# Optimization experiments

Measured on AMD Instinct MI355X. Metric: run time of the kernel, lower is better.

## Reference

```python
import jax, jax.numpy as jnp
import numpy as np

WH, WW = 7, 7
N = WH * WW
NH = 6
HEAD_DIM = 192 // NH
W_RES = 56
R_MAX = 4 * 56  # patch_size[0] * H
PI = 3.141592653589793


def _rel_coords():
    ch, cw = np.arange(WH), np.arange(WW)
    coords = np.stack(np.meshgrid(ch, cw, indexing='ij'))  # (2, WH, WW)
    flat = coords.reshape(2, -1)
    rel = flat[:, :, None] - flat[:, None, :]  # (2, N, N)
    radius = rel[0]   # in [-(WH-1), WH-1]
    azimuth = rel[1]  # in [-(WW-1), WW-1]
    return radius, azimuth


def setup_inputs() -> dict:
    key = jax.random.key(0)
    ks = jax.random.split(key, 10)
    B_ = 2048
    dim = 192
    return {
        'x': jax.random.normal(ks[0], (B_, N, dim), jnp.float32),
        'D': jax.random.uniform(ks[1], (B_, 1), jnp.float32),
        'qkv_w': jax.random.normal(ks[2], (3 * dim, dim), jnp.float32) * 0.02,
        'qkv_b': jax.random.normal(ks[3], (3 * dim,), jnp.float32) * 0.02,
        'proj_w': jax.random.normal(ks[4], (dim, dim), jnp.float32) * 0.02,
        'proj_b': jax.random.normal(ks[5], (dim,), jnp.float32) * 0.02,
        'a_p': jax.random.normal(ks[6], (2 * WW - 1, NH), jnp.float32) * 0.02,
        'b_p': jax.random.normal(ks[7], (2 * WW - 1, NH), jnp.float32) * 0.02,
        'a_r': jax.random.normal(ks[8], (2 * WH - 1, NH), jnp.float32) * 0.02,
        'b_r': jax.random.normal(ks[9], (2 * WH - 1, NH), jnp.float32) * 0.02,
    }


def reference(x, D, qkv_w, qkv_b, proj_w, proj_b, a_p, b_p, a_r, b_r):
    B_, n, C = x.shape
    radius_np, azimuth_np = _rel_coords()
    # torch a_r[radius] with negative ints wraps like python indexing; emulate via modulo
    rad_idx = jnp.asarray(radius_np % (2 * WH - 1))
    az_idx = jnp.asarray(azimuth_np % (2 * WW - 1))
    radius = jnp.asarray(radius_np, jnp.float32)   # (N, N)
    azimuth = jnp.asarray(azimuth_np, jnp.float32)  # (N, N)

    scale = HEAD_DIM ** -0.5
    qkv = (x @ qkv_w.T + qkv_b).reshape(B_, n, 3, NH, HEAD_DIM)
    qkv = jnp.transpose(qkv, (2, 0, 3, 1, 4))  # (3, B_, NH, N, hd)
    q, k, v = qkv[0] * scale, qkv[1], qkv[2]

    attn = jnp.einsum('bhnd,bhmd->bhnm', q, k)  # (B_, NH, N, N)

    # azimuthal bias: (N, N, NH) -> (NH, N, N)
    az = azimuth * (2.0 * PI / W_RES)
    A_phi = a_p[az_idx] * jnp.cos(az)[..., None] + b_p[az_idx] * jnp.sin(az)[..., None]
    A_phi = jnp.transpose(A_phi, (2, 0, 1))  # (NH, N, N)

    # radial bias: D (B_,1) scales radius -> (B_, N, N); combine -> (B_, NH, N, N)
    rad = D[:, 0][:, None, None] * radius[None]  # (B_, N, N)
    ang = rad * (2.0 * PI / R_MAX)
    A_r = (a_r[rad_idx][None] * jnp.cos(ang)[..., None]
           + b_r[rad_idx][None] * jnp.sin(ang)[..., None])  # (B_, N, N, NH)
    A_r = jnp.transpose(A_r, (0, 3, 1, 2))  # (B_, NH, N, N)

    attn = jax.nn.softmax(attn + A_phi[None] + A_r, axis=-1)
    out = jnp.einsum('bhnm,bhmd->bhnd', attn, v)
    out = jnp.transpose(out, (0, 2, 1, 3)).reshape(B_, n, C)
    return out @ proj_w.T + proj_b
```

## Files before the change

### kernel.cpp

```cpp
#include <hip/hip_runtime.h>

#define NTOK 49
#define NH 6
#define DIM 192
#define QKV_DIM 576
#define PI_F 3.14159265358979323846f
#define LOG2E_F 1.44269504088896340736f

typedef __bf16 bf16_t;
typedef __bf16 bf16x4 __attribute__((ext_vector_type(4)));
typedef __bf16 bf16x8 __attribute__((ext_vector_type(8)));
typedef float f32x4 __attribute__((ext_vector_type(4)));
typedef short s16x4 __attribute__((ext_vector_type(4)));

__global__ __launch_bounds__(256) void cvt_weights(const float* __restrict__ qkv_w,
                                                   const float* __restrict__ proj_w,
                                                   bf16_t* __restrict__ wq,
                                                   bf16_t* __restrict__ wp) {
    const float qscale = 0.17677669529663687f * LOG2E_F;
    int idx = blockIdx.x * 256 + threadIdx.x;
    if (idx < QKV_DIM * DIM) {
        float v = qkv_w[idx];
        if (idx < DIM * DIM) v *= qscale;
        wq[idx] = (bf16_t)v;
    } else {
        int j = idx - QKV_DIM * DIM;
        if (j < DIM * DIM) wp[j] = (bf16_t)proj_w[j];
    }
}

__device__ __forceinline__ int swz(int r, int c) {
    return r * DIM + (((c >> 3) ^ (r & 7)) << 3) + (c & 7);
}

__device__ __forceinline__ s16x4 pack4s(float a, float b, float c, float d) {
    bf16x4 t = { (bf16_t)a, (bf16_t)b, (bf16_t)c, (bf16_t)d };
    union { bf16x4 v; s16x4 s; } u;
    u.v = t;
    return u.s;
}

__global__ __launch_bounds__(768, 3) void fused_win_attn(
        const float* __restrict__ x,
        const float* __restrict__ Dp,
        const bf16_t* __restrict__ wq,
        const float* __restrict__ qkv_b,
        const bf16_t* __restrict__ wp,
        const float* __restrict__ proj_b,
        const float* __restrict__ a_p,
        const float* __restrict__ b_p,
        const float* __restrict__ a_r,
        const float* __restrict__ b_r,
        float* __restrict__ out,
        int nwin) {
    __shared__ __align__(16) bf16_t sh_xo[2][NTOK * DIM];
    __shared__ float bias_sh[12][170];

    const int tid  = threadIdx.x;
    const int w    = tid >> 6;
    const int lane = tid & 63;
    const int l16  = lane & 15;
    const int quad = lane >> 4;
    const int wb   = w / 6;
    const int h    = w % 6;
    const int win  = blockIdx.x * 2 + wb;
    const int winc = min(win, nwin - 1);
    const bool alive = (win < nwin);

    bf16_t* xl     = sh_xo[wb];
    float*  bias13 = bias_sh[w];

    for (int u = tid; u < 4704; u += 768) {
        int wbs = (u >= 2352) ? 1 : 0;
        int e = (u - wbs * 2352) * 4;
        int r = e / 192, c = e % 192;
        int wsrc = min(blockIdx.x * 2 + wbs, nwin - 1);
        float4 xv = *(const float4*)(x + (size_t)wsrc * (NTOK * DIM) + e);
        bf16x4 pk = { (bf16_t)xv.x, (bf16_t)xv.y, (bf16_t)xv.z, (bf16_t)xv.w };
        *(bf16x4*)(&sh_xo[wbs][swz(r, c)]) = pk;
    }

    const float Dv = Dp[winc];
    for (int u = lane; u < 170; u += 64) {
        if (u == 169) {
            bias13[u] = -1e30f;
        } else {
            int dr = u / 13 - 6, da = u % 13 - 6;
            int ri = (dr < 0) ? dr + 13 : dr;
            int ai = (da < 0) ? da + 13 : da;
            float ang_a = (float)da * (2.0f * PI_F / 56.0f);
            float ang_r = Dv * (float)dr * (2.0f * PI_F / 448.0f);
            bias13[u] = LOG2E_F *
                (a_p[ai * NH + h] * __cosf(ang_a) + b_p[ai * NH + h] * __sinf(ang_a)
               + a_r[ri * NH + h] * __cosf(ang_r) + b_r[ri * NH + h] * __sinf(ang_r));
        }
    }
    __syncthreads();

    int rowc[4];
#pragma unroll
    for (int mt = 0; mt < 4; ++mt)
        rowc[mt] = min(mt * 16 + l16, 48);

    s16x4 qp[4][2], kp[4][2], vp[4][2];
    {
        const bf16_t* wgq = wq + (size_t)(h * 32) * DIM;
        const bf16_t* wgk = wq + (size_t)(DIM + h * 32) * DIM;
        const bf16_t* wgv = wq + (size_t)(2 * DIM + h * 32) * DIM;
        f32x4 qa[4][2] = {}, ka[4][2] = {}, va[4][2] = {};
#pragma unroll
        for (int ks = 0; ks < 6; ++ks) {
            bf16x8 wq0 = *(const bf16x8*)(wgq + (size_t)l16 * DIM + ks * 32 + quad * 8);
            bf16x8 wq1 = *(const bf16x8*)(wgq + (size_t)(16 + l16) * DIM + ks * 32 + quad * 8);
            bf16x8 wk0 = *(const bf16x8*)(wgk + (size_t)l16 * DIM + ks * 32 + quad * 8);
            bf16x8 wk1 = *(const bf16x8*)(wgk + (size_t)(16 + l16) * DIM + ks * 32 + quad * 8);
            bf16x8 wv0 = *(const bf16x8*)(wgv + (size_t)l16 * DIM + ks * 32 + quad * 8);
            bf16x8 wv1 = *(const bf16x8*)(wgv + (size_t)(16 + l16) * DIM + ks * 32 + quad * 8);
#pragma unroll
            for (int mt = 0; mt < 4; ++mt) {
                bf16x8 xf = *(const bf16x8*)(&xl[swz(rowc[mt], ks * 32 + quad * 8)]);
                qa[mt][0] = __builtin_amdgcn_mfma_f32_16x16x32_bf16(wq0, xf, qa[mt][0], 0, 0, 0);
                qa[mt][1] = __builtin_amdgcn_mfma_f32_16x16x32_bf16(wq1, xf, qa[mt][1], 0, 0, 0);
                ka[mt][0] = __builtin_amdgcn_mfma_f32_16x16x32_bf16(wk0, xf, ka[mt][0], 0, 0, 0);
                ka[mt][1] = __builtin_amdgcn_mfma_f32_16x16x32_bf16(wk1, xf, ka[mt][1], 0, 0, 0);
                va[mt][0] = __builtin_amdgcn_mfma_f32_16x16x32_bf16(xf, wv0, va[mt][0], 0, 0, 0);
                va[mt][1] = __builtin_amdgcn_mfma_f32_16x16x32_bf16(xf, wv1, va[mt][1], 0, 0, 0);
            }
        }
        const float qbs = 0.17677669529663687f * LOG2E_F;
        float4 bq0 = *(const float4*)(qkv_b + h * 32 + quad * 4);
        float4 bq1 = *(const float4*)(qkv_b + h * 32 + 16 + quad * 4);
        float4 bk0 = *(const float4*)(qkv_b + DIM + h * 32 + quad * 4);
        float4 bk1 = *(const float4*)(qkv_b + DIM + h * 32 + 16 + quad * 4);
        float bv0 = qkv_b[2 * DIM + h * 32 + l16];
        float bv1 = qkv_b[2 * DIM + h * 32 + 16 + l16];
        float bq0x = bq0.x * qbs, bq0y = bq0.y * qbs, bq0z = bq0.z * qbs, bq0w = bq0.w * qbs;
        float bq1x = bq1.x * qbs, bq1y = bq1.y * qbs, bq1z = bq1.z * qbs, bq1w = bq1.w * qbs;
#pragma unroll
        for (int mt = 0; mt < 4; ++mt) {
            qp[mt][0] = pack4s(qa[mt][0][0] + bq0x, qa[mt][0][1] + bq0y,
                               qa[mt][0][2] + bq0z, qa[mt][0][3] + bq0w);
            qp[mt][1] = pack4s(qa[mt][1][0] + bq1x, qa[mt][1][1] + bq1y,
                               qa[mt][1][2] + bq1z, qa[mt][1][3] + bq1w);
            kp[mt][0] = pack4s(ka[mt][0][0] + bk0.x, ka[mt][0][1] + bk0.y,
                               ka[mt][0][2] + bk0.z, ka[mt][0][3] + bk0.w);
            kp[mt][1] = pack4s(ka[mt][1][0] + bk1.x, ka[mt][1][1] + bk1.y,
                               ka[mt][1][2] + bk1.z, ka[mt][1][3] + bk1.w);
            vp[mt][0] = pack4s(va[mt][0][0] + bv0, va[mt][0][1] + bv0,
                               va[mt][0][2] + bv0, va[mt][0][3] + bv0);
            vp[mt][1] = pack4s(va[mt][1][0] + bv1, va[mt][1][1] + bv1,
                               va[mt][1][2] + bv1, va[mt][1][3] + bv1);
        }
    }

    int jcp[4];
#pragma unroll
    for (int nt = 0; nt < 4; ++nt) {
        int p = 0;
#pragma unroll
        for (int r = 0; r < 4; ++r) {
            int j = nt * 16 + quad * 4 + r;
            int code = (j < 49) ? ((j / 7) * 13 + (j % 7)) : 240;
            p |= code << (8 * r);
        }
        jcp[nt] = p;
    }

    bf16x8 wf[2][6];
#pragma unroll
    for (int nt = 0; nt < 2; ++nt)
#pragma unroll
        for (int ks = 0; ks < 6; ++ks)
            wf[nt][ks] = *(const bf16x8*)(wp + (size_t)(h * 32 + nt * 16 + l16) * DIM + ks * 32 + quad * 8);

    __syncthreads();

    for (int mt = 0; mt < 4; ++mt) {
        f32x4 s[4] = {};
#pragma unroll
        for (int nt = 0; nt < 4; ++nt) {
            s[nt] = __builtin_amdgcn_mfma_f32_16x16x16bf16_1k(kp[nt][0], qp[mt][0], s[nt], 0, 0, 0);
            s[nt] = __builtin_amdgcn_mfma_f32_16x16x16bf16_1k(kp[nt][1], qp[mt][1], s[nt], 0, 0, 0);
        }

        int i = mt * 16 + l16;
        int icl = min(i, 48);
        int icode = (icl / 7) * 13 + (icl % 7) + 84;

        float ev[4][4];
        float sum = 0.f;
#pragma unroll
        for (int nt = 0; nt < 4; ++nt)
#pragma unroll
            for (int r = 0; r < 4; ++r) {
                unsigned idx = (unsigned)(icode - ((jcp[nt] >> (8 * r)) & 255));
                idx = min(idx, 169u);
                float e = __builtin_amdgcn_exp2f(s[nt][r] + bias13[idx]);
                ev[nt][r] = e;
                sum += e;
            }
        sum += __shfl_xor(sum, 16);
        sum += __shfl_xor(sum, 32);
        float rs = __builtin_amdgcn_rcpf(sum);

        s16x4 pvs[4];
#pragma unroll
        for (int nt = 0; nt < 4; ++nt)
            pvs[nt] = pack4s(ev[nt][0], ev[nt][1], ev[nt][2], ev[nt][3]);

        f32x4 o0 = {}, o1 = {};
#pragma unroll
        for (int kt = 0; kt < 4; ++kt) {
            o0 = __builtin_amdgcn_mfma_f32_16x16x16bf16_1k(vp[kt][0], pvs[kt], o0, 0, 0, 0);
            o1 = __builtin_amdgcn_mfma_f32_16x16x16bf16_1k(vp[kt][1], pvs[kt], o1, 0, 0, 0);
        }

        if (i < 49) {
            *(s16x4*)(&xl[swz(i, h * 32 + quad * 4)]) =
                pack4s(o0[0] * rs, o0[1] * rs, o0[2] * rs, o0[3] * rs);
            *(s16x4*)(&xl[swz(i, h * 32 + 16 + quad * 4)]) =
                pack4s(o1[0] * rs, o1[1] * rs, o1[2] * rs, o1[3] * rs);
        }
    }

    __syncthreads();

    f32x4 pacc[4][2] = {};
#pragma unroll
    for (int mt = 0; mt < 4; ++mt)
#pragma unroll
        for (int ks = 0; ks < 6; ++ks) {
            bf16x8 oa = *(const bf16x8*)(&xl[swz(rowc[mt], ks * 32 + quad * 8)]);
            pacc[mt][0] = __builtin_amdgcn_mfma_f32_16x16x32_bf16(oa, wf[0][ks], pacc[mt][0], 0, 0, 0);
            pacc[mt][1] = __builtin_amdgcn_mfma_f32_16x16x32_bf16(oa, wf[1][ks], pacc[mt][1], 0, 0, 0);
        }

    float pb0 = proj_b[h * 32 + l16];
    float pb1 = proj_b[h * 32 + 16 + l16];
#pragma unroll
    for (int mt = 0; mt < 4; ++mt)
#pragma unroll
        for (int r = 0; r < 4; ++r) {
            int i = mt * 16 + quad * 4 + r;
            if (alive && i < 49) {
                float* op = out + ((size_t)win * NTOK + i) * DIM + h * 32;
                op[l16]      = pacc[mt][0][r] + pb0;
                op[16 + l16] = pacc[mt][1][r] + pb1;
            }
        }
}

extern "C" void kernel_launch(void* const* d_in, const int* in_sizes, int n_in,
                              void* d_out, int out_size, void* d_ws, size_t ws_size,
                              hipStream_t stream) {
    const float* x      = (const float*)d_in[0];
    const float* D      = (const float*)d_in[1];
    const float* qkv_w  = (const float*)d_in[2];
    const float* qkv_b  = (const float*)d_in[3];
    const float* proj_w = (const float*)d_in[4];
    const float* proj_b = (const float*)d_in[5];
    const float* a_p    = (const float*)d_in[6];
    const float* b_p    = (const float*)d_in[7];
    const float* a_r    = (const float*)d_in[8];
    const float* b_r    = (const float*)d_in[9];
    float* out = (float*)d_out;

    const int B_ = in_sizes[0] / (NTOK * DIM);

    char* wsp = (char*)d_ws;
    bf16_t* wq = (bf16_t*)wsp; wsp += (size_t)QKV_DIM * DIM * 2;
    bf16_t* wp = (bf16_t*)wsp;

    cvt_weights<<<dim3((QKV_DIM * DIM + DIM * DIM + 255) / 256), dim3(256), 0, stream>>>(
        qkv_w, proj_w, wq, wp);

    fused_win_attn<<<dim3((B_ + 1) / 2), dim3(768), 0, stream>>>(
        x, D, wq, qkv_b, wp, proj_b, a_p, b_p, a_r, b_r, out, B_);
}
```

Measured before the change: 263.7 us.

## Make attention kernel persistent and keep QKV weight fragments in registers

The fused window-attention kernel becomes persistent. The grid is capped at 512 blocks, and each block loops over window pairs. The QKV weight fragments and the bias values are loaded into registers once per block and reused across iterations instead of being reloaded for every pair. The aim is to cut repeated weight fetches and per-block setup. In exchange it holds many more live registers, which risks spills, and it adds an extra barrier per iteration. The capped grid may also leave fewer resident blocks per CU than before.

```diff
diff --git a/kernel.cpp b/kernel.cpp
--- a/kernel.cpp
+++ b/kernel.cpp
@@ -40,7 +40,7 @@
     return u.s;
 }
 
-__global__ __launch_bounds__(768, 3) void fused_win_attn(
+__global__ __launch_bounds__(768, 6) void fused_win_attn(
         const float* __restrict__ x,
         const float* __restrict__ Dp,
         const bf16_t* __restrict__ wq,
@@ -63,95 +63,30 @@
     const int quad = lane >> 4;
     const int wb   = w / 6;
     const int h    = w % 6;
-    const int win  = blockIdx.x * 2 + wb;
-    const int winc = min(win, nwin - 1);
-    const bool alive = (win < nwin);
 
     bf16_t* xl     = sh_xo[wb];
     float*  bias13 = bias_sh[w];
 
-    for (int u = tid; u < 4704; u += 768) {
-        int wbs = (u >= 2352) ? 1 : 0;
-        int e = (u - wbs * 2352) * 4;
-        int r = e / 192, c = e % 192;
-        int wsrc = min(blockIdx.x * 2 + wbs, nwin - 1);
-        float4 xv = *(const float4*)(x + (size_t)wsrc * (NTOK * DIM) + e);
-        bf16x4 pk = { (bf16_t)xv.x, (bf16_t)xv.y, (bf16_t)xv.z, (bf16_t)xv.w };
-        *(bf16x4*)(&sh_xo[wbs][swz(r, c)]) = pk;
-    }
-
-    const float Dv = Dp[winc];
-    for (int u = lane; u < 170; u += 64) {
-        if (u == 169) {
-            bias13[u] = -1e30f;
-        } else {
-            int dr = u / 13 - 6, da = u % 13 - 6;
-            int ri = (dr < 0) ? dr + 13 : dr;
-            int ai = (da < 0) ? da + 13 : da;
-            float ang_a = (float)da * (2.0f * PI_F / 56.0f);
-            float ang_r = Dv * (float)dr * (2.0f * PI_F / 448.0f);
-            bias13[u] = LOG2E_F *
-                (a_p[ai * NH + h] * __cosf(ang_a) + b_p[ai * NH + h] * __sinf(ang_a)
-               + a_r[ri * NH + h] * __cosf(ang_r) + b_r[ri * NH + h] * __sinf(ang_r));
-        }
-    }
-    __syncthreads();
-
-    int rowc[4];
-#pragma unroll
-    for (int mt = 0; mt < 4; ++mt)
-        rowc[mt] = min(mt * 16 + l16, 48);
-
-    s16x4 qp[4][2], kp[4][2], vp[4][2];
+    bf16x8 wfq[6][2], wfk[6][2], wfv[6][2];
     {
         const bf16_t* wgq = wq + (size_t)(h * 32) * DIM;
         const bf16_t* wgk = wq + (size_t)(DIM + h * 32) * DIM;
         const bf16_t* wgv = wq + (size_t)(2 * DIM + h * 32) * DIM;
-        f32x4 qa[4][2] = {}, ka[4][2] = {}, va[4][2] = {};
 #pragma unroll
         for (int ks = 0; ks < 6; ++ks) {
-            bf16x8 wq0 = *(const bf16x8*)(wgq + (size_t)l16 * DIM + ks * 32 + quad * 8);
-            bf16x8 wq1 = *(const bf16x8*)(wgq + (size_t)(16 + l16) * DIM + ks * 32 + quad * 8);
-            bf16x8 wk0 = *(const bf16x8*)(wgk + (size_t)l16 * DIM + ks * 32 + quad * 8);
-            bf16x8 wk1 = *(const bf16x8*)(wgk + (size_t)(16 + l16) * DIM + ks * 32 + quad * 8);
-            bf16x8 wv0 = *(const bf16x8*)(wgv + (size_t)l16 * DIM + ks * 32 + quad * 8);
-            bf16x8 wv1 = *(const bf16x8*)(wgv + (size_t)(16 + l16) * DIM + ks * 32 + quad * 8);
-#pragma unroll
-            for (int mt = 0; mt < 4; ++mt) {
-                bf16x8 xf = *(const bf16x8*)(&xl[swz(rowc[mt], ks * 32 + quad * 8)]);
-                qa[mt][0] = __builtin_amdgcn_mfma_f32_16x16x32_bf16(wq0, xf, qa[mt][0], 0, 0, 0);
-                qa[mt][1] = __builtin_amdgcn_mfma_f32_16x16x32_bf16(wq1, xf, qa[mt][1], 0, 0, 0);
-                ka[mt][0] = __builtin_amdgcn_mfma_f32_16x16x32_bf16(wk0, xf, ka[mt][0], 0, 0, 0);
-                ka[mt][1] = __builtin_amdgcn_mfma_f32_16x16x32_bf16(wk1, xf, ka[mt][1], 0, 0, 0);
-                va[mt][0] = __builtin_amdgcn_mfma_f32_16x16x32_bf16(xf, wv0, va[mt][0], 0, 0, 0);
-                va[mt][1] = __builtin_amdgcn_mfma_f32_16x16x32_bf16(xf, wv1, va[mt][1], 0, 0, 0);
-            }
-        }
-        const float qbs = 0.17677669529663687f * LOG2E_F;
-        float4 bq0 = *(const float4*)(qkv_b + h * 32 + quad * 4);
-        float4 bq1 = *(const float4*)(qkv_b + h * 32 + 16 + quad * 4);
-        float4 bk0 = *(const float4*)(qkv_b + DIM + h * 32 + quad * 4);
-        float4 bk1 = *(const float4*)(qkv_b + DIM + h * 32 + 16 + quad * 4);
-        float bv0 = qkv_b[2 * DIM + h * 32 + l16];
-        float bv1 = qkv_b[2 * DIM + h * 32 + 16 + l16];
-        float bq0x = bq0.x * qbs, bq0y = bq0.y * qbs, bq0z = bq0.z * qbs, bq0w = bq0.w * qbs;
-        float bq1x = bq1.x * qbs, bq1y = bq1.y * qbs, bq1z = bq1.z * qbs, bq1w = bq1.w * qbs;
-#pragma unroll
-        for (int mt = 0; mt < 4; ++mt) {
-            qp[mt][0] = pack4s(qa[mt][0][0] + bq0x, qa[mt][0][1] + bq0y,
-                               qa[mt][0][2] + bq0z, qa[mt][0][3] + bq0w);
-            qp[mt][1] = pack4s(qa[mt][1][0] + bq1x, qa[mt][1][1] + bq1y,
-                               qa[mt][1][2] + bq1z, qa[mt][1][3] + bq1w);
-            kp[mt][0] = pack4s(ka[mt][0][0] + bk0.x, ka[mt][0][1] + bk0.y,
-                               ka[mt][0][2] + bk0.z, ka[mt][0][3] + bk0.w);
-            kp[mt][1] = pack4s(ka[mt][1][0] + bk1.x, ka[mt][1][1] + bk1.y,
-                               ka[mt][1][2] + bk1.z, ka[mt][1][3] + bk1.w);
-            vp[mt][0] = pack4s(va[mt][0][0] + bv0, va[mt][0][1] + bv0,
-                               va[mt][0][2] + bv0, va[mt][0][3] + bv0);
-            vp[mt][1] = pack4s(va[mt][1][0] + bv1, va[mt][1][1] + bv1,
-                               va[mt][1][2] + bv1, va[mt][1][3] + bv1);
-        }
-    }
+            wfq[ks][0] = *(const bf16x8*)(wgq + (size_t)l16 * DIM + ks * 32 + quad * 8);
+            wfq[ks][1] = *(const bf16x8*)(wgq + (size_t)(16 + l16) * DIM + ks * 32 + quad * 8);
+            wfk[ks][0] = *(const bf16x8*)(wgk + (size_t)l16 * DIM + ks * 32 + quad * 8);
+            wfk[ks][1] = *(const bf16x8*)(wgk + (size_t)(16 + l16) * DIM + ks * 32 + quad * 8);
+            wfv[ks][0] = *(const bf16x8*)(wgv + (size_t)l16 * DIM + ks * 32 + quad * 8);
+            wfv[ks][1] = *(const bf16x8*)(wgv + (size_t)(16 + l16) * DIM + ks * 32 + quad * 8);
+        }
+    }
+
+    int rowc[4];
+#pragma unroll
+    for (int mt = 0; mt < 4; ++mt)
+        rowc[mt] = min(mt * 16 + l16, 48);
 
     int jcp[4];
 #pragma unroll
@@ -166,88 +101,167 @@
         jcp[nt] = p;
     }
 
-    bf16x8 wf[2][6];
-#pragma unroll
-    for (int nt = 0; nt < 2; ++nt)
-#pragma unroll
-        for (int ks = 0; ks < 6; ++ks)
-            wf[nt][ks] = *(const bf16x8*)(wp + (size_t)(h * 32 + nt * 16 + l16) * DIM + ks * 32 + quad * 8);
-
-    __syncthreads();
-
-    for (int mt = 0; mt < 4; ++mt) {
-        f32x4 s[4] = {};
-#pragma unroll
-        for (int nt = 0; nt < 4; ++nt) {
-            s[nt] = __builtin_amdgcn_mfma_f32_16x16x16bf16_1k(kp[nt][0], qp[mt][0], s[nt], 0, 0, 0);
-            s[nt] = __builtin_amdgcn_mfma_f32_16x16x16bf16_1k(kp[nt][1], qp[mt][1], s[nt], 0, 0, 0);
-        }
-
-        int i = mt * 16 + l16;
-        int icl = min(i, 48);
-        int icode = (icl / 7) * 13 + (icl % 7) + 84;
-
-        float ev[4][4];
-        float sum = 0.f;
-#pragma unroll
-        for (int nt = 0; nt < 4; ++nt)
+    const float qbs = 0.17677669529663687f * LOG2E_F;
+    float4 bq0 = *(const float4*)(qkv_b + h * 32 + quad * 4);
+    float4 bq1 = *(const float4*)(qkv_b + h * 32 + 16 + quad * 4);
+    float4 bk0 = *(const float4*)(qkv_b + DIM + h * 32 + quad * 4);
+    float4 bk1 = *(const float4*)(qkv_b + DIM + h * 32 + 16 + quad * 4);
+    const float bv0 = qkv_b[2 * DIM + h * 32 + l16];
+    const float bv1 = qkv_b[2 * DIM + h * 32 + 16 + l16];
+    const float bq0x = bq0.x * qbs, bq0y = bq0.y * qbs, bq0z = bq0.z * qbs, bq0w = bq0.w * qbs;
+    const float bq1x = bq1.x * qbs, bq1y = bq1.y * qbs, bq1z = bq1.z * qbs, bq1w = bq1.w * qbs;
+    const float pb0 = proj_b[h * 32 + l16];
+    const float pb1 = proj_b[h * 32 + 16 + l16];
+
+    const int npairs = (nwin + 1) >> 1;
+    for (int pair = blockIdx.x; pair < npairs; pair += gridDim.x) {
+        const int win  = pair * 2 + wb;
+        const int winc = min(win, nwin - 1);
+        const bool alive = (win < nwin);
+
+        for (int u = tid; u < 4704; u += 768) {
+            int wbs = (u >= 2352) ? 1 : 0;
+            int e = (u - wbs * 2352) * 4;
+            int r = e / 192, c = e % 192;
+            int wsrc = min(pair * 2 + wbs, nwin - 1);
+            float4 xv = *(const float4*)(x + (size_t)wsrc * (NTOK * DIM) + e);
+            bf16x4 pk = { (bf16_t)xv.x, (bf16_t)xv.y, (bf16_t)xv.z, (bf16_t)xv.w };
+            *(bf16x4*)(&sh_xo[wbs][swz(r, c)]) = pk;
+        }
+
+        const float Dv = Dp[winc];
+        for (int u = lane; u < 170; u += 64) {
+            if (u == 169) {
+                bias13[u] = -1e30f;
+            } else {
+                int dr = u / 13 - 6, da = u % 13 - 6;
+                int ri = (dr < 0) ? dr + 13 : dr;
+                int ai = (da < 0) ? da + 13 : da;
+                float ang_a = (float)da * (2.0f * PI_F / 56.0f);
+                float ang_r = Dv * (float)dr * (2.0f * PI_F / 448.0f);
+                bias13[u] = LOG2E_F *
+                    (a_p[ai * NH + h] * __cosf(ang_a) + b_p[ai * NH + h] * __sinf(ang_a)
+                   + a_r[ri * NH + h] * __cosf(ang_r) + b_r[ri * NH + h] * __sinf(ang_r));
+            }
+        }
+        __syncthreads();
+
+        s16x4 qp[4][2], kp[4][2], vp[4][2];
+        {
+            f32x4 qa[4][2] = {}, ka[4][2] = {}, va[4][2] = {};
+#pragma unroll
+            for (int ks = 0; ks < 6; ++ks) {
+#pragma unroll
+                for (int mt = 0; mt < 4; ++mt) {
+                    bf16x8 xf = *(const bf16x8*)(&xl[swz(rowc[mt], ks * 32 + quad * 8)]);
+                    qa[mt][0] = __builtin_amdgcn_mfma_f32_16x16x32_bf16(wfq[ks][0], xf, qa[mt][0], 0, 0, 0);
+                    qa[mt][1] = __builtin_amdgcn_mfma_f32_16x16x32_bf16(wfq[ks][1], xf, qa[mt][1], 0, 0, 0);
+                    ka[mt][0] = __builtin_amdgcn_mfma_f32_16x16x32_bf16(wfk[ks][0], xf, ka[mt][0], 0, 0, 0);
+                    ka[mt][1] = __builtin_amdgcn_mfma_f32_16x16x32_bf16(wfk[ks][1], xf, ka[mt][1], 0, 0, 0);
+                    va[mt][0] = __builtin_amdgcn_mfma_f32_16x16x32_bf16(xf, wfv[ks][0], va[mt][0], 0, 0, 0);
+                    va[mt][1] = __builtin_amdgcn_mfma_f32_16x16x32_bf16(xf, wfv[ks][1], va[mt][1], 0, 0, 0);
+                }
+            }
+#pragma unroll
+            for (int mt = 0; mt < 4; ++mt) {
+                qp[mt][0] = pack4s(qa[mt][0][0] + bq0x, qa[mt][0][1] + bq0y,
+                                   qa[mt][0][2] + bq0z, qa[mt][0][3] + bq0w);
+                qp[mt][1] = pack4s(qa[mt][1][0] + bq1x, qa[mt][1][1] + bq1y,
+                                   qa[mt][1][2] + bq1z, qa[mt][1][3] + bq1w);
+                kp[mt][0] = pack4s(ka[mt][0][0] + bk0.x, ka[mt][0][1] + bk0.y,
+                                   ka[mt][0][2] + bk0.z, ka[mt][0][3] + bk0.w);
+                kp[mt][1] = pack4s(ka[mt][1][0] + bk1.x, ka[mt][1][1] + bk1.y,
+                                   ka[mt][1][2] + bk1.z, ka[mt][1][3] + bk1.w);
+                vp[mt][0] = pack4s(va[mt][0][0] + bv0, va[mt][0][1] + bv0,
+                                   va[mt][0][2] + bv0, va[mt][0][3] + bv0);
+                vp[mt][1] = pack4s(va[mt][1][0] + bv1, va[mt][1][1] + bv1,
+                                   va[mt][1][2] + bv1, va[mt][1][3] + bv1);
+            }
+        }
+
+        bf16x8 wf[2][6];
+#pragma unroll
+        for (int nt = 0; nt < 2; ++nt)
+#pragma unroll
+            for (int ks = 0; ks < 6; ++ks)
+                wf[nt][ks] = *(const bf16x8*)(wp + (size_t)(h * 32 + nt * 16 + l16) * DIM + ks * 32 + quad * 8);
+
+        __syncthreads();
+
+        for (int mt = 0; mt < 4; ++mt) {
+            f32x4 s[4] = {};
+#pragma unroll
+            for (int nt = 0; nt < 4; ++nt) {
+                s[nt] = __builtin_amdgcn_mfma_f32_16x16x16bf16_1k(kp[nt][0], qp[mt][0], s[nt], 0, 0, 0);
+                s[nt] = __builtin_amdgcn_mfma_f32_16x16x16bf16_1k(kp[nt][1], qp[mt][1], s[nt], 0, 0, 0);
+            }
+
+            int i = mt * 16 + l16;
+            int icl = min(i, 48);
+            int icode = (icl / 7) * 13 + (icl % 7) + 84;
+
+            float ev[4][4];
+            float sum = 0.f;
+#pragma unroll
+            for (int nt = 0; nt < 4; ++nt)
+#pragma unroll
+                for (int r = 0; r < 4; ++r) {
+                    unsigned idx = (unsigned)(icode - ((jcp[nt] >> (8 * r)) & 255));
+                    idx = min(idx, 169u);
+                    float e = __builtin_amdgcn_exp2f(s[nt][r] + bias13[idx]);
+                    ev[nt][r] = e;
+                    sum += e;
+                }
+            sum += __shfl_xor(sum, 16);
+            sum += __shfl_xor(sum, 32);
+            float rs = __builtin_amdgcn_rcpf(sum);
+
+            s16x4 pvs[4];
+#pragma unroll
+            for (int nt = 0; nt < 4; ++nt)
+                pvs[nt] = pack4s(ev[nt][0], ev[nt][1], ev[nt][2], ev[nt][3]);
+
+            f32x4 o0 = {}, o1 = {};
+#pragma unroll
+            for (int kt = 0; kt < 4; ++kt) {
+                o0 = __builtin_amdgcn_mfma_f32_16x16x16bf16_1k(vp[kt][0], pvs[kt], o0, 0, 0, 0);
+                o1 = __builtin_amdgcn_mfma_f32_16x16x16bf16_1k(vp[kt][1], pvs[kt], o1, 0, 0, 0);
+            }
+
+            if (i < 49) {
+                *(s16x4*)(&xl[swz(i, h * 32 + quad * 4)]) =
+                    pack4s(o0[0] * rs, o0[1] * rs, o0[2] * rs, o0[3] * rs);
+                *(s16x4*)(&xl[swz(i, h * 32 + 16 + quad * 4)]) =
+                    pack4s(o1[0] * rs, o1[1] * rs, o1[2] * rs, o1[3] * rs);
+            }
+        }
+
+        __syncthreads();
+
+        f32x4 pacc[4][2] = {};
+#pragma unroll
+        for (int mt = 0; mt < 4; ++mt)
+#pragma unroll
+            for (int ks = 0; ks < 6; ++ks) {
+                bf16x8 oa = *(const bf16x8*)(&xl[swz(rowc[mt], ks * 32 + quad * 8)]);
+                pacc[mt][0] = __builtin_amdgcn_mfma_f32_16x16x32_bf16(oa, wf[0][ks], pacc[mt][0], 0, 0, 0);
+                pacc[mt][1] = __builtin_amdgcn_mfma_f32_16x16x32_bf16(oa, wf[1][ks], pacc[mt][1], 0, 0, 0);
+            }
+
+#pragma unroll
+        for (int mt = 0; mt < 4; ++mt)
 #pragma unroll
             for (int r = 0; r < 4; ++r) {
-                unsigned idx = (unsigned)(icode - ((jcp[nt] >> (8 * r)) & 255));
-                idx = min(idx, 169u);
-                float e = __builtin_amdgcn_exp2f(s[nt][r] + bias13[idx]);
-                ev[nt][r] = e;
-                sum += e;
-            }
-        sum += __shfl_xor(sum, 16);
-        sum += __shfl_xor(sum, 32);
-        float rs = __builtin_amdgcn_rcpf(sum);
-
-        s16x4 pvs[4];
-#pragma unroll
-        for (int nt = 0; nt < 4; ++nt)
-            pvs[nt] = pack4s(ev[nt][0], ev[nt][1], ev[nt][2], ev[nt][3]);
-
-        f32x4 o0 = {}, o1 = {};
-#pragma unroll
-        for (int kt = 0; kt < 4; ++kt) {
-            o0 = __builtin_amdgcn_mfma_f32_16x16x16bf16_1k(vp[kt][0], pvs[kt], o0, 0, 0, 0);
-            o1 = __builtin_amdgcn_mfma_f32_16x16x16bf16_1k(vp[kt][1], pvs[kt], o1, 0, 0, 0);
-        }
-
-        if (i < 49) {
-            *(s16x4*)(&xl[swz(i, h * 32 + quad * 4)]) =
-                pack4s(o0[0] * rs, o0[1] * rs, o0[2] * rs, o0[3] * rs);
-            *(s16x4*)(&xl[swz(i, h * 32 + 16 + quad * 4)]) =
-                pack4s(o1[0] * rs, o1[1] * rs, o1[2] * rs, o1[3] * rs);
-        }
-    }
-
-    __syncthreads();
-
-    f32x4 pacc[4][2] = {};
-#pragma unroll
-    for (int mt = 0; mt < 4; ++mt)
-#pragma unroll
-        for (int ks = 0; ks < 6; ++ks) {
-            bf16x8 oa = *(const bf16x8*)(&xl[swz(rowc[mt], ks * 32 + quad * 8)]);
-            pacc[mt][0] = __builtin_amdgcn_mfma_f32_16x16x32_bf16(oa, wf[0][ks], pacc[mt][0], 0, 0, 0);
-            pacc[mt][1] = __builtin_amdgcn_mfma_f32_16x16x32_bf16(oa, wf[1][ks], pacc[mt][1], 0, 0, 0);
-        }
-
-    float pb0 = proj_b[h * 32 + l16];
-    float pb1 = proj_b[h * 32 + 16 + l16];
-#pragma unroll
-    for (int mt = 0; mt < 4; ++mt)
-#pragma unroll
-        for (int r = 0; r < 4; ++r) {
-            int i = mt * 16 + quad * 4 + r;
-            if (alive && i < 49) {
-                float* op = out + ((size_t)win * NTOK + i) * DIM + h * 32;
-                op[l16]      = pacc[mt][0][r] + pb0;
-                op[16 + l16] = pacc[mt][1][r] + pb1;
-            }
-        }
+                int i = mt * 16 + quad * 4 + r;
+                if (alive && i < 49) {
+                    float* op = out + ((size_t)win * NTOK + i) * DIM + h * 32;
+                    op[l16]      = pacc[mt][0][r] + pb0;
+                    op[16 + l16] = pacc[mt][1][r] + pb1;
+                }
+            }
+
+        __syncthreads();
+    }
 }
 
 extern "C" void kernel_launch(void* const* d_in, const int* in_sizes, int n_in,
@@ -274,6 +288,8 @@
     cvt_weights<<<dim3((QKV_DIM * DIM + DIM * DIM + 255) / 256), dim3(256), 0, stream>>>(
         qkv_w, proj_w, wq, wp);
 
-    fused_win_attn<<<dim3((B_ + 1) / 2), dim3(768), 0, stream>>>(
+    const int npairs = (B_ + 1) / 2;
+    const int grid = npairs < 512 ? npairs : 512;
+    fused_win_attn<<<dim3(grid), dim3(768), 0, stream>>>(
         x, D, wq, qkv_b, wp, proj_b, a_p, b_p, a_r, b_r, out, B_);
 }
```

After: 895.8 us. 240% more time.

## Make attention kernel persistent with async global-to-LDS prefetch of next window pair

Applied to the files above, without the earlier changes.

Converts the per-window-pair launch into a persistent kernel capped at 256 blocks that loops over window pairs. Each pair's x tile is prefetched with global_load_lds into a new fp32 staging buffer while the current pair is computed, then converted to bf16 in LDS after the loop body. The aim is to hide global load latency behind MFMA work. In exchange it adds about 75KB of LDS, which lowers occupancy (launch bounds still ask for 3 blocks per CU), and it relies on hand-placed waitcnt and barriers for correctness.

```diff
diff --git a/kernel.cpp b/kernel.cpp
--- a/kernel.cpp
+++ b/kernel.cpp
@@ -54,6 +54,7 @@
         float* __restrict__ out,
         int nwin) {
     __shared__ __align__(16) bf16_t sh_xo[2][NTOK * DIM];
+    __shared__ __align__(16) float  stage32[18816];
     __shared__ float bias_sh[12][170];
 
     const int tid  = threadIdx.x;
@@ -63,95 +64,50 @@
     const int quad = lane >> 4;
     const int wb   = w / 6;
     const int h    = w % 6;
-    const int win  = blockIdx.x * 2 + wb;
-    const int winc = min(win, nwin - 1);
-    const bool alive = (win < nwin);
 
     bf16_t* xl     = sh_xo[wb];
     float*  bias13 = bias_sh[w];
 
-    for (int u = tid; u < 4704; u += 768) {
-        int wbs = (u >= 2352) ? 1 : 0;
-        int e = (u - wbs * 2352) * 4;
-        int r = e / 192, c = e % 192;
-        int wsrc = min(blockIdx.x * 2 + wbs, nwin - 1);
-        float4 xv = *(const float4*)(x + (size_t)wsrc * (NTOK * DIM) + e);
-        bf16x4 pk = { (bf16_t)xv.x, (bf16_t)xv.y, (bf16_t)xv.z, (bf16_t)xv.w };
-        *(bf16x4*)(&sh_xo[wbs][swz(r, c)]) = pk;
-    }
-
-    const float Dv = Dp[winc];
-    for (int u = lane; u < 170; u += 64) {
-        if (u == 169) {
-            bias13[u] = -1e30f;
-        } else {
-            int dr = u / 13 - 6, da = u % 13 - 6;
-            int ri = (dr < 0) ? dr + 13 : dr;
-            int ai = (da < 0) ? da + 13 : da;
-            float ang_a = (float)da * (2.0f * PI_F / 56.0f);
-            float ang_r = Dv * (float)dr * (2.0f * PI_F / 448.0f);
-            bias13[u] = LOG2E_F *
-                (a_p[ai * NH + h] * __cosf(ang_a) + b_p[ai * NH + h] * __sinf(ang_a)
-               + a_r[ri * NH + h] * __cosf(ang_r) + b_r[ri * NH + h] * __sinf(ang_r));
-        }
-    }
-    __syncthreads();
+    auto stage_issue = [&](int p) {
+#pragma unroll
+        for (int u = 0; u < 7; ++u) {
+            int idx = u * 768 + tid;
+            if (idx < 4704) {
+                int wbs = idx >= 2352;
+                int e   = idx - wbs * 2352;
+                int wsrc = min(p * 2 + wbs, nwin - 1);
+                const float* gp = x + (size_t)wsrc * (NTOK * DIM) + (size_t)e * 4;
+                float* lp = &stage32[(idx & ~63) * 4];
+                __builtin_amdgcn_global_load_lds(
+                    (const __attribute__((address_space(1))) void*)gp,
+                    (__attribute__((address_space(3))) void*)lp, 16, 0, 0);
+            }
+        }
+    };
+
+    auto convert_stage = [&]() {
+#pragma unroll
+        for (int u = 0; u < 7; ++u) {
+            int idx = u * 768 + tid;
+            if (idx < 4704) {
+                int wbs = idx >= 2352;
+                int e   = (idx - wbs * 2352) * 4;
+                int r = e / 192, c = e % 192;
+                float4 xv = *(const float4*)(&stage32[idx * 4]);
+                bf16x4 pk = { (bf16_t)xv.x, (bf16_t)xv.y, (bf16_t)xv.z, (bf16_t)xv.w };
+                *(bf16x4*)(&sh_xo[wbs][swz(r, c)]) = pk;
+            }
+        }
+    };
+
+    const int npairs = (nwin + 1) >> 1;
+
+    stage_issue(blockIdx.x);
 
     int rowc[4];
 #pragma unroll
     for (int mt = 0; mt < 4; ++mt)
         rowc[mt] = min(mt * 16 + l16, 48);
-
-    s16x4 qp[4][2], kp[4][2], vp[4][2];
-    {
-        const bf16_t* wgq = wq + (size_t)(h * 32) * DIM;
-        const bf16_t* wgk = wq + (size_t)(DIM + h * 32) * DIM;
-        const bf16_t* wgv = wq + (size_t)(2 * DIM + h * 32) * DIM;
-        f32x4 qa[4][2] = {}, ka[4][2] = {}, va[4][2] = {};
-#pragma unroll
-        for (int ks = 0; ks < 6; ++ks) {
-            bf16x8 wq0 = *(const bf16x8*)(wgq + (size_t)l16 * DIM + ks * 32 + quad * 8);
-            bf16x8 wq1 = *(const bf16x8*)(wgq + (size_t)(16 + l16) * DIM + ks * 32 + quad * 8);
-            bf16x8 wk0 = *(const bf16x8*)(wgk + (size_t)l16 * DIM + ks * 32 + quad * 8);
-            bf16x8 wk1 = *(const bf16x8*)(wgk + (size_t)(16 + l16) * DIM + ks * 32 + quad * 8);
-            bf16x8 wv0 = *(const bf16x8*)(wgv + (size_t)l16 * DIM + ks * 32 + quad * 8);
-            bf16x8 wv1 = *(const bf16x8*)(wgv + (size_t)(16 + l16) * DIM + ks * 32 + quad * 8);
-#pragma unroll
-            for (int mt = 0; mt < 4; ++mt) {
-                bf16x8 xf = *(const bf16x8*)(&xl[swz(rowc[mt], ks * 32 + quad * 8)]);
-                qa[mt][0] = __builtin_amdgcn_mfma_f32_16x16x32_bf16(wq0, xf, qa[mt][0], 0, 0, 0);
-                qa[mt][1] = __builtin_amdgcn_mfma_f32_16x16x32_bf16(wq1, xf, qa[mt][1], 0, 0, 0);
-                ka[mt][0] = __builtin_amdgcn_mfma_f32_16x16x32_bf16(wk0, xf, ka[mt][0], 0, 0, 0);
-                ka[mt][1] = __builtin_amdgcn_mfma_f32_16x16x32_bf16(wk1, xf, ka[mt][1], 0, 0, 0);
-                va[mt][0] = __builtin_amdgcn_mfma_f32_16x16x32_bf16(xf, wv0, va[mt][0], 0, 0, 0);
-                va[mt][1] = __builtin_amdgcn_mfma_f32_16x16x32_bf16(xf, wv1, va[mt][1], 0, 0, 0);
-            }
-        }
-        const float qbs = 0.17677669529663687f * LOG2E_F;
-        float4 bq0 = *(const float4*)(qkv_b + h * 32 + quad * 4);
-        float4 bq1 = *(const float4*)(qkv_b + h * 32 + 16 + quad * 4);
-        float4 bk0 = *(const float4*)(qkv_b + DIM + h * 32 + quad * 4);
-        float4 bk1 = *(const float4*)(qkv_b + DIM + h * 32 + 16 + quad * 4);
-        float bv0 = qkv_b[2 * DIM + h * 32 + l16];
-        float bv1 = qkv_b[2 * DIM + h * 32 + 16 + l16];
-        float bq0x = bq0.x * qbs, bq0y = bq0.y * qbs, bq0z = bq0.z * qbs, bq0w = bq0.w * qbs;
-        float bq1x = bq1.x * qbs, bq1y = bq1.y * qbs, bq1z = bq1.z * qbs, bq1w = bq1.w * qbs;
-#pragma unroll
-        for (int mt = 0; mt < 4; ++mt) {
-            qp[mt][0] = pack4s(qa[mt][0][0] + bq0x, qa[mt][0][1] + bq0y,
-                               qa[mt][0][2] + bq0z, qa[mt][0][3] + bq0w);
-            qp[mt][1] = pack4s(qa[mt][1][0] + bq1x, qa[mt][1][1] + bq1y,
-                               qa[mt][1][2] + bq1z, qa[mt][1][3] + bq1w);
-            kp[mt][0] = pack4s(ka[mt][0][0] + bk0.x, ka[mt][0][1] + bk0.y,
-                               ka[mt][0][2] + bk0.z, ka[mt][0][3] + bk0.w);
-            kp[mt][1] = pack4s(ka[mt][1][0] + bk1.x, ka[mt][1][1] + bk1.y,
-                               ka[mt][1][2] + bk1.z, ka[mt][1][3] + bk1.w);
-            vp[mt][0] = pack4s(va[mt][0][0] + bv0, va[mt][0][1] + bv0,
-                               va[mt][0][2] + bv0, va[mt][0][3] + bv0);
-            vp[mt][1] = pack4s(va[mt][1][0] + bv1, va[mt][1][1] + bv1,
-                               va[mt][1][2] + bv1, va[mt][1][3] + bv1);
-        }
-    }
 
     int jcp[4];
 #pragma unroll
@@ -166,88 +122,174 @@
         jcp[nt] = p;
     }
 
-    bf16x8 wf[2][6];
-#pragma unroll
-    for (int nt = 0; nt < 2; ++nt)
-#pragma unroll
-        for (int ks = 0; ks < 6; ++ks)
-            wf[nt][ks] = *(const bf16x8*)(wp + (size_t)(h * 32 + nt * 16 + l16) * DIM + ks * 32 + quad * 8);
+    const float qbs = 0.17677669529663687f * LOG2E_F;
+    float4 bq0 = *(const float4*)(qkv_b + h * 32 + quad * 4);
+    float4 bq1 = *(const float4*)(qkv_b + h * 32 + 16 + quad * 4);
+    float4 bk0 = *(const float4*)(qkv_b + DIM + h * 32 + quad * 4);
+    float4 bk1 = *(const float4*)(qkv_b + DIM + h * 32 + 16 + quad * 4);
+    const float bv0 = qkv_b[2 * DIM + h * 32 + l16];
+    const float bv1 = qkv_b[2 * DIM + h * 32 + 16 + l16];
+    const float bq0x = bq0.x * qbs, bq0y = bq0.y * qbs, bq0z = bq0.z * qbs, bq0w = bq0.w * qbs;
+    const float bq1x = bq1.x * qbs, bq1y = bq1.y * qbs, bq1z = bq1.z * qbs, bq1w = bq1.w * qbs;
+    const float pb0 = proj_b[h * 32 + l16];
+    const float pb1 = proj_b[h * 32 + 16 + l16];
 
     __syncthreads();
-
-    for (int mt = 0; mt < 4; ++mt) {
-        f32x4 s[4] = {};
-#pragma unroll
-        for (int nt = 0; nt < 4; ++nt) {
-            s[nt] = __builtin_amdgcn_mfma_f32_16x16x16bf16_1k(kp[nt][0], qp[mt][0], s[nt], 0, 0, 0);
-            s[nt] = __builtin_amdgcn_mfma_f32_16x16x16bf16_1k(kp[nt][1], qp[mt][1], s[nt], 0, 0, 0);
-        }
-
-        int i = mt * 16 + l16;
-        int icl = min(i, 48);
-        int icode = (icl / 7) * 13 + (icl % 7) + 84;
-
-        float ev[4][4];
-        float sum = 0.f;
-#pragma unroll
-        for (int nt = 0; nt < 4; ++nt)
+    convert_stage();
+    asm volatile("s_waitcnt lgkmcnt(0)" ::: "memory");
+    __builtin_amdgcn_s_barrier();
+
+    for (int pair = blockIdx.x; pair < npairs; pair += gridDim.x) {
+        const int nxt  = pair + gridDim.x;
+        const int win  = pair * 2 + wb;
+        const int winc = min(win, nwin - 1);
+        const bool alive = (win < nwin);
+
+        if (nxt < npairs) stage_issue(nxt);
+
+        const float Dv = Dp[winc];
+        for (int u = lane; u < 170; u += 64) {
+            if (u == 169) {
+                bias13[u] = -1e30f;
+            } else {
+                int dr = u / 13 - 6, da = u % 13 - 6;
+                int ri = (dr < 0) ? dr + 13 : dr;
+                int ai = (da < 0) ? da + 13 : da;
+                float ang_a = (float)da * (2.0f * PI_F / 56.0f);
+                float ang_r = Dv * (float)dr * (2.0f * PI_F / 448.0f);
+                bias13[u] = LOG2E_F *
+                    (a_p[ai * NH + h] * __cosf(ang_a) + b_p[ai * NH + h] * __sinf(ang_a)
+                   + a_r[ri * NH + h] * __cosf(ang_r) + b_r[ri * NH + h] * __sinf(ang_r));
+            }
+        }
+
+        s16x4 qp[4][2], kp[4][2], vp[4][2];
+        {
+            const bf16_t* wgq = wq + (size_t)(h * 32) * DIM;
+            const bf16_t* wgk = wq + (size_t)(DIM + h * 32) * DIM;
+            const bf16_t* wgv = wq + (size_t)(2 * DIM + h * 32) * DIM;
+            f32x4 qa[4][2] = {}, ka[4][2] = {}, va[4][2] = {};
+#pragma unroll
+            for (int ks = 0; ks < 6; ++ks) {
+                bf16x8 wq0 = *(const bf16x8*)(wgq + (size_t)l16 * DIM + ks * 32 + quad * 8);
+                bf16x8 wq1 = *(const bf16x8*)(wgq + (size_t)(16 + l16) * DIM + ks * 32 + quad * 8);
+                bf16x8 wk0 = *(const bf16x8*)(wgk + (size_t)l16 * DIM + ks * 32 + quad * 8);
+                bf16x8 wk1 = *(const bf16x8*)(wgk + (size_t)(16 + l16) * DIM + ks * 32 + quad * 8);
+                bf16x8 wv0 = *(const bf16x8*)(wgv + (size_t)l16 * DIM + ks * 32 + quad * 8);
+                bf16x8 wv1 = *(const bf16x8*)(wgv + (size_t)(16 + l16) * DIM + ks * 32 + quad * 8);
+#pragma unroll
+                for (int mt = 0; mt < 4; ++mt) {
+                    bf16x8 xf = *(const bf16x8*)(&xl[swz(rowc[mt], ks * 32 + quad * 8)]);
+                    qa[mt][0] = __builtin_amdgcn_mfma_f32_16x16x32_bf16(wq0, xf, qa[mt][0], 0, 0, 0);
+                    qa[mt][1] = __builtin_amdgcn_mfma_f32_16x16x32_bf16(wq1, xf, qa[mt][1], 0, 0, 0);
+                    ka[mt][0] = __builtin_amdgcn_mfma_f32_16x16x32_bf16(wk0, xf, ka[mt][0], 0, 0, 0);
+                    ka[mt][1] = __builtin_amdgcn_mfma_f32_16x16x32_bf16(wk1, xf, ka[mt][1], 0, 0, 0);
+                    va[mt][0] = __builtin_amdgcn_mfma_f32_16x16x32_bf16(xf, wv0, va[mt][0], 0, 0, 0);
+                    va[mt][1] = __builtin_amdgcn_mfma_f32_16x16x32_bf16(xf, wv1, va[mt][1], 0, 0, 0);
+                }
+            }
+#pragma unroll
+            for (int mt = 0; mt < 4; ++mt) {
+                qp[mt][0] = pack4s(qa[mt][0][0] + bq0x, qa[mt][0][1] + bq0y,
+                                   qa[mt][0][2] + bq0z, qa[mt][0][3] + bq0w);
+                qp[mt][1] = pack4s(qa[mt][1][0] + bq1x, qa[mt][1][1] + bq1y,
+                                   qa[mt][1][2] + bq1z, qa[mt][1][3] + bq1w);
+                kp[mt][0] = pack4s(ka[mt][0][0] + bk0.x, ka[mt][0][1] + bk0.y,
+                                   ka[mt][0][2] + bk0.z, ka[mt][0][3] + bk0.w);
+                kp[mt][1] = pack4s(ka[mt][1][0] + bk1.x, ka[mt][1][1] + bk1.y,
+                                   ka[mt][1][2] + bk1.z, ka[mt][1][3] + bk1.w);
+                vp[mt][0] = pack4s(va[mt][0][0] + bv0, va[mt][0][1] + bv0,
+                                   va[mt][0][2] + bv0, va[mt][0][3] + bv0);
+                vp[mt][1] = pack4s(va[mt][1][0] + bv1, va[mt][1][1] + bv1,
+                                   va[mt][1][2] + bv1, va[mt][1][3] + bv1);
+            }
+        }
+
+        bf16x8 wf[2][6];
+#pragma unroll
+        for (int nt = 0; nt < 2; ++nt)
+#pragma unroll
+            for (int ks = 0; ks < 6; ++ks)
+                wf[nt][ks] = *(const bf16x8*)(wp + (size_t)(h * 32 + nt * 16 + l16) * DIM + ks * 32 + quad * 8);
+
+        __builtin_amdgcn_s_barrier();
+
+        for (int mt = 0; mt < 4; ++mt) {
+            f32x4 s[4] = {};
+#pragma unroll
+            for (int nt = 0; nt < 4; ++nt) {
+                s[nt] = __builtin_amdgcn_mfma_f32_16x16x16bf16_1k(kp[nt][0], qp[mt][0], s[nt], 0, 0, 0);
+                s[nt] = __builtin_amdgcn_mfma_f32_16x16x16bf16_1k(kp[nt][1], qp[mt][1], s[nt], 0, 0, 0);
+            }
+
+            int i = mt * 16 + l16;
+            int icl = min(i, 48);
+            int icode = (icl / 7) * 13 + (icl % 7) + 84;
+
+            float sum = 0.f;
+            s16x4 pvs[4];
+#pragma unroll
+            for (int nt = 0; nt < 4; ++nt) {
+                unsigned i0 = min((unsigned)(icode - ( jcp[nt]        & 255)), 169u);
+                unsigned i1 = min((unsigned)(icode - ((jcp[nt] >>  8) & 255)), 169u);
+                unsigned i2 = min((unsigned)(icode - ((jcp[nt] >> 16) & 255)), 169u);
+                unsigned i3 = min((unsigned)(icode - ((jcp[nt] >> 24) & 255)), 169u);
+                float e0 = __builtin_amdgcn_exp2f(s[nt][0] + bias13[i0]);
+                float e1 = __builtin_amdgcn_exp2f(s[nt][1] + bias13[i1]);
+                float e2 = __builtin_amdgcn_exp2f(s[nt][2] + bias13[i2]);
+                float e3 = __builtin_amdgcn_exp2f(s[nt][3] + bias13[i3]);
+                sum += (e0 + e1) + (e2 + e3);
+                pvs[nt] = pack4s(e0, e1, e2, e3);
+            }
+            sum += __shfl_xor(sum, 16);
+            sum += __shfl_xor(sum, 32);
+            float rs = __builtin_amdgcn_rcpf(sum);
+
+            f32x4 o0 = {}, o1 = {};
+#pragma unroll
+            for (int kt = 0; kt < 4; ++kt) {
+                o0 = __builtin_amdgcn_mfma_f32_16x16x16bf16_1k(vp[kt][0], pvs[kt], o0, 0, 0, 0);
+                o1 = __builtin_amdgcn_mfma_f32_16x16x16bf16_1k(vp[kt][1], pvs[kt], o1, 0, 0, 0);
+            }
+
+            if (i < 49) {
+                *(s16x4*)(&xl[swz(i, h * 32 + quad * 4)]) =
+                    pack4s(o0[0] * rs, o0[1] * rs, o0[2] * rs, o0[3] * rs);
+                *(s16x4*)(&xl[swz(i, h * 32 + 16 + quad * 4)]) =
+                    pack4s(o1[0] * rs, o1[1] * rs, o1[2] * rs, o1[3] * rs);
+            }
+        }
+
+        asm volatile("s_waitcnt lgkmcnt(0)" ::: "memory");
+        __builtin_amdgcn_s_barrier();
+
+        f32x4 pacc[4][2] = {};
+#pragma unroll
+        for (int mt = 0; mt < 4; ++mt)
+#pragma unroll
+            for (int ks = 0; ks < 6; ++ks) {
+                bf16x8 oa = *(const bf16x8*)(&xl[swz(rowc[mt], ks * 32 + quad * 8)]);
+                pacc[mt][0] = __builtin_amdgcn_mfma_f32_16x16x32_bf16(oa, wf[0][ks], pacc[mt][0], 0, 0, 0);
+                pacc[mt][1] = __builtin_amdgcn_mfma_f32_16x16x32_bf16(oa, wf[1][ks], pacc[mt][1], 0, 0, 0);
+            }
+
+#pragma unroll
+        for (int mt = 0; mt < 4; ++mt)
 #pragma unroll
             for (int r = 0; r < 4; ++r) {
-                unsigned idx = (unsigned)(icode - ((jcp[nt] >> (8 * r)) & 255));
-                idx = min(idx, 169u);
-                float e = __builtin_amdgcn_exp2f(s[nt][r] + bias13[idx]);
-                ev[nt][r] = e;
-                sum += e;
-            }
-        sum += __shfl_xor(sum, 16);
-        sum += __shfl_xor(sum, 32);
-        float rs = __builtin_amdgcn_rcpf(sum);
-
-        s16x4 pvs[4];
-#pragma unroll
-        for (int nt = 0; nt < 4; ++nt)
-            pvs[nt] = pack4s(ev[nt][0], ev[nt][1], ev[nt][2], ev[nt][3]);
-
-        f32x4 o0 = {}, o1 = {};
-#pragma unroll
-        for (int kt = 0; kt < 4; ++kt) {
-            o0 = __builtin_amdgcn_mfma_f32_16x16x16bf16_1k(vp[kt][0], pvs[kt], o0, 0, 0, 0);
-            o1 = __builtin_amdgcn_mfma_f32_16x16x16bf16_1k(vp[kt][1], pvs[kt], o1, 0, 0, 0);
-        }
-
-        if (i < 49) {
-            *(s16x4*)(&xl[swz(i, h * 32 + quad * 4)]) =
-                pack4s(o0[0] * rs, o0[1] * rs, o0[2] * rs, o0[3] * rs);
-            *(s16x4*)(&xl[swz(i, h * 32 + 16 + quad * 4)]) =
-                pack4s(o1[0] * rs, o1[1] * rs, o1[2] * rs, o1[3] * rs);
-        }
+                int i = mt * 16 + quad * 4 + r;
+                if (alive && i < 49) {
+                    float* op = out + ((size_t)win * NTOK + i) * DIM + h * 32;
+                    op[l16]      = pacc[mt][0][r] + pb0;
+                    op[16 + l16] = pacc[mt][1][r] + pb1;
+                }
+            }
+
+        __syncthreads();
+        if (nxt < npairs) convert_stage();
+        asm volatile("s_waitcnt lgkmcnt(0)" ::: "memory");
+        __builtin_amdgcn_s_barrier();
     }
-
-    __syncthreads();
-
-    f32x4 pacc[4][2] = {};
-#pragma unroll
-    for (int mt = 0; mt < 4; ++mt)
-#pragma unroll
-        for (int ks = 0; ks < 6; ++ks) {
-            bf16x8 oa = *(const bf16x8*)(&xl[swz(rowc[mt], ks * 32 + quad * 8)]);
-            pacc[mt][0] = __builtin_amdgcn_mfma_f32_16x16x32_bf16(oa, wf[0][ks], pacc[mt][0], 0, 0, 0);
-            pacc[mt][1] = __builtin_amdgcn_mfma_f32_16x16x32_bf16(oa, wf[1][ks], pacc[mt][1], 0, 0, 0);
-        }
-
-    float pb0 = proj_b[h * 32 + l16];
-    float pb1 = proj_b[h * 32 + 16 + l16];
-#pragma unroll
-    for (int mt = 0; mt < 4; ++mt)
-#pragma unroll
-        for (int r = 0; r < 4; ++r) {
-            int i = mt * 16 + quad * 4 + r;
-            if (alive && i < 49) {
-                float* op = out + ((size_t)win * NTOK + i) * DIM + h * 32;
-                op[l16]      = pacc[mt][0][r] + pb0;
-                op[16 + l16] = pacc[mt][1][r] + pb1;
-            }
-        }
 }
 
 extern "C" void kernel_launch(void* const* d_in, const int* in_sizes, int n_in,
@@ -274,6 +316,8 @@
     cvt_weights<<<dim3((QKV_DIM * DIM + DIM * DIM + 255) / 256), dim3(256), 0, stream>>>(
         qkv_w, proj_w, wq, wp);
 
-    fused_win_attn<<<dim3((B_ + 1) / 2), dim3(768), 0, stream>>>(
+    const int npairs = (B_ + 1) / 2;
+    const int grid = npairs < 256 ? npairs : 256;
+    fused_win_attn<<<dim3(grid), dim3(768), 0, stream>>>(
         x, D, wq, qkv_b, wp, proj_b, a_p, b_p, a_r, b_r, out, B_);
 }
```

Result: slower. 556.1 us (+110.9%).
